# Optimization experiments

Hardware: AMD Instinct MI355X
Metric: run time of the kernel (lower is better)

The kernel has to match this reference:

```python
import jax, jax.numpy as jnp
import numpy as np

N = 50000
E = 800000
D_IN = 128
D_OUT = 128
LN_EPS = 1e-5
DROP_P = 0.1


def setup_inputs() -> dict:
    key = jax.random.key(0)
    ks = jax.random.split(key, 8)
    x = jax.random.normal(ks[0], (N, D_IN), dtype=jnp.float32)
    edge_index = jax.random.randint(ks[1], (2, E), 0, N, dtype=jnp.int64)
    # dropout mask: binary keep-mask scaled by 1/(1-p), as torch dropout produces
    u = jax.random.uniform(ks[2], (N, D_IN), dtype=jnp.float32)
    dropout_mask = (u > DROP_P).astype(jnp.float32) / (1.0 - DROP_P)
    # LayerNorm affine params
    gamma = jnp.ones((D_IN,), dtype=jnp.float32)
    beta = jnp.zeros((D_IN,), dtype=jnp.float32)
    # SAGEConv linears: lin_l (aggregated neighbors, with bias), lin_r (root, no bias)
    s = 1.0 / np.sqrt(D_IN)
    w_l = jax.random.uniform(ks[3], (D_OUT, D_IN), minval=-s, maxval=s, dtype=jnp.float32)
    b_l = jax.random.uniform(ks[4], (D_OUT,), minval=-s, maxval=s, dtype=jnp.float32)
    w_r = jax.random.uniform(ks[5], (D_OUT, D_IN), minval=-s, maxval=s, dtype=jnp.float32)
    return {"x": x, "edge_index": edge_index, "dropout_mask": dropout_mask,
            "gamma": gamma, "beta": beta, "w_l": w_l, "b_l": b_l, "w_r": w_r}


def reference(x, edge_index, dropout_mask, gamma, beta, w_l, b_l, w_r):
    # LayerNorm + ReLU + dropout mask
    mu = jnp.mean(x, axis=-1, keepdims=True)
    var = jnp.mean(jnp.square(x - mu), axis=-1, keepdims=True)
    h = (x - mu) * jax.lax.rsqrt(var + LN_EPS) * gamma + beta
    h = jax.nn.relu(h) * dropout_mask  # [N, D_IN]
    # SAGEConv: mean-aggregate source features into target nodes
    src = edge_index[0]
    dst = edge_index[1]
    msg = h[src]  # [E, D_IN] gathered messages
    agg = jax.ops.segment_sum(msg, dst, num_segments=N)  # [N, D_IN]
    deg = jax.ops.segment_sum(jnp.ones((E,), dtype=h.dtype), dst, num_segments=N)
    agg = agg / jnp.maximum(deg, 1.0)[:, None]
    # out = lin_l(agg) + lin_r(h)
    out = agg @ w_l.T + b_l + h @ w_r.T  # [N, D_OUT]
    return out
```

## Files before the change

### kernel.cpp

```cpp
#include <hip/hip_runtime.h>
#include <hip/hip_bf16.h>

#define N_NODES 50000
#define N_EDGES 800000
#define D 128
#define NB_SCAN ((N_NODES + 255) / 256)
#define NB_GEMM ((N_NODES + 63) / 64)
#define EDGES_PER_GEMM_BLOCK 1024

typedef short bf16x8 __attribute__((ext_vector_type(8)));
typedef float f32x4 __attribute__((ext_vector_type(4)));

__device__ __forceinline__ unsigned int bf16u(float f) {
  __hip_bfloat16 b = __float2bfloat16(f);
  return (unsigned int)*reinterpret_cast<unsigned short*>(&b);
}

__global__ __launch_bounds__(256) void zero_kernel(int* __restrict__ deg,
                                                   int* __restrict__ done) {
  const int i = blockIdx.x * 256 + threadIdx.x;
  if (i < N_NODES) deg[i] = 0;
  if (i == 0) *done = 0;
}

__global__ __launch_bounds__(256) void gemm_kernel(
    const float* __restrict__ x, const float* __restrict__ mask,
    const float* __restrict__ gamma, const float* __restrict__ beta,
    const float* __restrict__ w_l, const float* __restrict__ w_r,
    const float* __restrict__ b_l, unsigned int* __restrict__ gb,
    float* __restrict__ rp, const int* __restrict__ ei,
    int* __restrict__ deg, int* __restrict__ rank) {
  __shared__ unsigned short Bs[64 * 64 * 8];
  const int t = threadIdx.x;
  const int w = t >> 6;
  const int l = t & 63;
  const int lm = l & 15;
  const int quad = l >> 4;
  const int nb = blockIdx.x * 64;

  {
    const int e = blockIdx.x * EDGES_PER_GEMM_BLOCK + t * 4;
    if (e + 3 < N_EDGES) {
      const int4 d4 = *(const int4*)(ei + N_EDGES + e);
      int4 r4;
      r4.x = atomicAdd(&deg[d4.x], 1);
      r4.y = atomicAdd(&deg[d4.y], 1);
      r4.z = atomicAdd(&deg[d4.z], 1);
      r4.w = atomicAdd(&deg[d4.w], 1);
      *(int4*)(rank + e) = r4;
    } else {
      for (int k = e; k < N_EDGES; ++k)
        rank[k] = atomicAdd(&deg[ei[N_EDGES + k]], 1);
    }
  }

#pragma unroll
  for (int i = 0; i < 16; ++i) {
    const int fid = w * 16 + i;
    const int sub = fid >> 2;
    const int ch = fid & 3;
    const float* srcw = (sub < 8) ? (w_l + (size_t)(sub * 16 + lm) * D)
                                  : (w_r + (size_t)((sub - 8) * 16 + lm) * D);
    const float4 a = *(const float4*)(srcw + ch * 32 + quad * 8);
    const float4 b = *(const float4*)(srcw + ch * 32 + quad * 8 + 4);
    uint4 v;
    v.x = (bf16u(a.y) << 16) | bf16u(a.x);
    v.y = (bf16u(a.w) << 16) | bf16u(a.z);
    v.z = (bf16u(b.y) << 16) | bf16u(b.x);
    v.w = (bf16u(b.w) << 16) | bf16u(b.z);
    *(uint4*)(Bs + ((size_t)fid * 64 + l) * 8) = v;
  }

  int anode = nb + w * 16 + lm;
  if (anode >= N_NODES) anode = N_NODES - 1;
  const float* xrow = x + (size_t)anode * D;
  float xv[32];
  float s = 0.f, q = 0.f;
#pragma unroll
  for (int ch = 0; ch < 4; ++ch) {
    const float4 a = *(const float4*)(xrow + ch * 32 + quad * 8);
    const float4 b = *(const float4*)(xrow + ch * 32 + quad * 8 + 4);
    xv[ch * 8 + 0] = a.x; xv[ch * 8 + 1] = a.y;
    xv[ch * 8 + 2] = a.z; xv[ch * 8 + 3] = a.w;
    xv[ch * 8 + 4] = b.x; xv[ch * 8 + 5] = b.y;
    xv[ch * 8 + 6] = b.z; xv[ch * 8 + 7] = b.w;
    s += (a.x + a.y) + (a.z + a.w) + (b.x + b.y) + (b.z + b.w);
    q += a.x * a.x + a.y * a.y + a.z * a.z + a.w * a.w +
         b.x * b.x + b.y * b.y + b.z * b.z + b.w * b.w;
  }
  s += __shfl_xor(s, 16);
  s += __shfl_xor(s, 32);
  q += __shfl_xor(q, 16);
  q += __shfl_xor(q, 32);
  const float mean = s * (1.0f / 128.0f);
  const float var = q * (1.0f / 128.0f) - mean * mean;
  const float rs = rsqrtf(var + 1e-5f);

  const float* mrow = mask + (size_t)anode * D;
  bf16x8 af[4];
#pragma unroll
  for (int ch = 0; ch < 4; ++ch) {
    const int c0 = ch * 32 + quad * 8;
    const float4 g0 = *(const float4*)(gamma + c0);
    const float4 g1 = *(const float4*)(gamma + c0 + 4);
    const float4 b0 = *(const float4*)(beta + c0);
    const float4 b1 = *(const float4*)(beta + c0 + 4);
    const float4 m0 = *(const float4*)(mrow + c0);
    const float4 m1 = *(const float4*)(mrow + c0 + 4);
    const float gv[8] = {g0.x, g0.y, g0.z, g0.w, g1.x, g1.y, g1.z, g1.w};
    const float bv[8] = {b0.x, b0.y, b0.z, b0.w, b1.x, b1.y, b1.z, b1.w};
    const float mv[8] = {m0.x, m0.y, m0.z, m0.w, m1.x, m1.y, m1.z, m1.w};
#pragma unroll
    for (int j = 0; j < 8; ++j) {
      const float hv =
          fmaxf((xv[ch * 8 + j] - mean) * rs * gv[j] + bv[j], 0.0f) * mv[j];
      af[ch][j] = (short)bf16u(hv);
    }
  }
  __syncthreads();

  f32x4 acc[16];
#pragma unroll
  for (int sub = 0; sub < 16; ++sub) acc[sub] = (f32x4){0.f, 0.f, 0.f, 0.f};
  const bf16x8* BsF = (const bf16x8*)Bs;
#pragma unroll
  for (int sub = 0; sub < 16; ++sub)
#pragma unroll
    for (int ch = 0; ch < 4; ++ch)
      acc[sub] = __builtin_amdgcn_mfma_f32_16x16x32_bf16(
          af[ch], BsF[(sub * 4 + ch) * 64 + l], acc[sub], 0, 0, 0);

  float blv[8];
#pragma unroll
  for (int j = 0; j < 8; ++j) blv[j] = b_l[j * 16 + lm];

  const int node0 = nb + w * 16 + quad * 4;
#pragma unroll
  for (int reg = 0; reg < 4; ++reg) {
    const int node = node0 + reg;
    if (node < N_NODES) {
      uint4 p;
      p.x = (bf16u(acc[1][reg]) << 16) | bf16u(acc[0][reg]);
      p.y = (bf16u(acc[3][reg]) << 16) | bf16u(acc[2][reg]);
      p.z = (bf16u(acc[5][reg]) << 16) | bf16u(acc[4][reg]);
      p.w = (bf16u(acc[7][reg]) << 16) | bf16u(acc[6][reg]);
      ((uint4*)gb)[(size_t)node * 16 + lm] = p;
      float4 q0, q1;
      q0.x = acc[8][reg] + blv[0];
      q0.y = acc[9][reg] + blv[1];
      q0.z = acc[10][reg] + blv[2];
      q0.w = acc[11][reg] + blv[3];
      q1.x = acc[12][reg] + blv[4];
      q1.y = acc[13][reg] + blv[5];
      q1.z = acc[14][reg] + blv[6];
      q1.w = acc[15][reg] + blv[7];
      ((float4*)rp)[(size_t)node * 32 + lm * 2 + 0] = q0;
      ((float4*)rp)[(size_t)node * 32 + lm * 2 + 1] = q1;
    }
  }
}

__global__ __launch_bounds__(256) void scan12_kernel(
    const int* __restrict__ deg, int* __restrict__ offL1,
    int* __restrict__ partial, int* __restrict__ partial2,
    int* __restrict__ done) {
  __shared__ int sm[256];
  __shared__ int amLast;
  const int t = threadIdx.x;
  const int i = blockIdx.x * 256 + t;
  const int v = (i < N_NODES) ? deg[i] : 0;
  sm[t] = v;
  __syncthreads();
#pragma unroll
  for (int ofs = 1; ofs < 256; ofs <<= 1) {
    int x = sm[t];
    if (t >= ofs) x += sm[t - ofs];
    __syncthreads();
    sm[t] = x;
    __syncthreads();
  }
  if (i < N_NODES) offL1[i] = sm[t] - v;
  if (t == 255)
    __hip_atomic_store(&partial[blockIdx.x], sm[255], __ATOMIC_RELEASE,
                       __HIP_MEMORY_SCOPE_AGENT);
  __syncthreads();
  if (t == 0) amLast = (atomicAdd(done, 1) == gridDim.x - 1);
  __syncthreads();
  if (amLast) {
    const int pv = (t < NB_SCAN)
                       ? __hip_atomic_load(&partial[t], __ATOMIC_ACQUIRE,
                                           __HIP_MEMORY_SCOPE_AGENT)
                       : 0;
    sm[t] = pv;
    __syncthreads();
#pragma unroll
    for (int ofs = 1; ofs < 256; ofs <<= 1) {
      int x = sm[t];
      if (t >= ofs) x += sm[t - ofs];
      __syncthreads();
      sm[t] = x;
      __syncthreads();
    }
    if (t < NB_SCAN) partial2[t] = sm[t] - pv;
  }
}

__global__ __launch_bounds__(256) void scatter_kernel(
    const int* __restrict__ ei, const int* __restrict__ offL1,
    const int* __restrict__ partial2, const int* __restrict__ rank,
    int* __restrict__ csr) {
  const int e = (blockIdx.x * 256 + threadIdx.x) * 4;
  if (e + 3 < N_EDGES) {
    const int4 s4 = *(const int4*)(ei + e);
    const int4 d4 = *(const int4*)(ei + N_EDGES + e);
    const int4 r4 = *(const int4*)(rank + e);
    csr[offL1[d4.x] + partial2[d4.x >> 8] + r4.x] = s4.x;
    csr[offL1[d4.y] + partial2[d4.y >> 8] + r4.y] = s4.y;
    csr[offL1[d4.z] + partial2[d4.z >> 8] + r4.z] = s4.z;
    csr[offL1[d4.w] + partial2[d4.w >> 8] + r4.w] = s4.w;
  } else {
    for (int k = e; k < N_EDGES; ++k) {
      const int dst = ei[N_EDGES + k];
      csr[offL1[dst] + partial2[dst >> 8] + rank[k]] = ei[k];
    }
  }
}

#define ACC8(v)                                     \
  do {                                              \
    acc[0] += __uint_as_float((v).x << 16);         \
    acc[1] += __uint_as_float((v).x & 0xffff0000u); \
    acc[2] += __uint_as_float((v).y << 16);         \
    acc[3] += __uint_as_float((v).y & 0xffff0000u); \
    acc[4] += __uint_as_float((v).z << 16);         \
    acc[5] += __uint_as_float((v).z & 0xffff0000u); \
    acc[6] += __uint_as_float((v).w << 16);         \
    acc[7] += __uint_as_float((v).w & 0xffff0000u); \
  } while (0)

__global__ __launch_bounds__(256) void agg_kernel(
    const int* __restrict__ offL1, const int* __restrict__ partial2,
    const int* __restrict__ csr, const unsigned int* __restrict__ gb,
    const float* __restrict__ rp, float* __restrict__ out) {
  const int l = threadIdx.x & 63;
  const int q = l >> 4;
  const int c = l & 15;
  const int n = blockIdx.x * 4 + (threadIdx.x >> 6);
  const int s = offL1[n] + partial2[n >> 8];
  const int e = (n + 1 < N_NODES) ? offL1[n + 1] + partial2[(n + 1) >> 8]
                                  : N_EDGES;
  const uint4* g4 = (const uint4*)gb;
  float acc[8];
#pragma unroll
  for (int k = 0; k < 8; ++k) acc[k] = 0.0f;
  for (int base = s; base < e; base += 64) {
    const int cnt = min(e - base, 64);
    int idx = (l < cnt) ? csr[base + l] : 0;
    int j = 0;
    for (; j + 16 <= cnt; j += 16) {
      const int i0 = __shfl(idx, j + 0 + q);
      const int i1 = __shfl(idx, j + 4 + q);
      const int i2 = __shfl(idx, j + 8 + q);
      const int i3 = __shfl(idx, j + 12 + q);
      const uint4 v0 = g4[(size_t)i0 * 16 + c];
      const uint4 v1 = g4[(size_t)i1 * 16 + c];
      const uint4 v2 = g4[(size_t)i2 * 16 + c];
      const uint4 v3 = g4[(size_t)i3 * 16 + c];
      ACC8(v0);
      ACC8(v1);
      ACC8(v2);
      ACC8(v3);
    }
    for (; j + 4 <= cnt; j += 4) {
      const int i0 = __shfl(idx, j + q);
      const uint4 v0 = g4[(size_t)i0 * 16 + c];
      ACC8(v0);
    }
    if (j < cnt) {
      const int rem = cnt - j;
      const int i0 = __shfl(idx, j + min(q, rem - 1));
      if (q < rem) {
        const uint4 v0 = g4[(size_t)i0 * 16 + c];
        ACC8(v0);
      }
    }
  }
#pragma unroll
  for (int k = 0; k < 8; ++k) {
    acc[k] += __shfl_xor(acc[k], 16);
    acc[k] += __shfl_xor(acc[k], 32);
  }
  if (l < 16) {
    const float inv = 1.0f / fmaxf((float)(e - s), 1.0f);
    const float4 rp0 = ((const float4*)rp)[(size_t)n * 32 + c * 2 + 0];
    const float4 rp1 = ((const float4*)rp)[(size_t)n * 32 + c * 2 + 1];
    float* o = out + (size_t)n * D + c;
    o[0]   = fmaf(acc[0], inv, rp0.x);
    o[16]  = fmaf(acc[1], inv, rp0.y);
    o[32]  = fmaf(acc[2], inv, rp0.z);
    o[48]  = fmaf(acc[3], inv, rp0.w);
    o[64]  = fmaf(acc[4], inv, rp1.x);
    o[80]  = fmaf(acc[5], inv, rp1.y);
    o[96]  = fmaf(acc[6], inv, rp1.z);
    o[112] = fmaf(acc[7], inv, rp1.w);
  }
}

extern "C" void kernel_launch(void* const* d_in, const int* in_sizes, int n_in,
                              void* d_out, int out_size, void* d_ws,
                              size_t ws_size, hipStream_t stream) {
  const float* x = (const float*)d_in[0];
  const int* ei = (const int*)d_in[1];
  const float* mask = (const float*)d_in[2];
  const float* gamma = (const float*)d_in[3];
  const float* beta = (const float*)d_in[4];
  const float* w_l = (const float*)d_in[5];
  const float* b_l = (const float*)d_in[6];
  const float* w_r = (const float*)d_in[7];
  float* out = (float*)d_out;

  char* ws = (char*)d_ws;
  size_t off = 0;
  auto alloc = [&](size_t bytes) {
    char* p = ws + off;
    off += (bytes + 255) & ~(size_t)255;
    return p;
  };
  unsigned int* gb =
      (unsigned int*)alloc((size_t)N_NODES * D * sizeof(unsigned short));
  float* rp = (float*)alloc((size_t)N_NODES * D * sizeof(float));
  int* deg = (int*)alloc((size_t)N_NODES * sizeof(int));
  int* offL1 = (int*)alloc((size_t)N_NODES * sizeof(int));
  int* partial = (int*)alloc((size_t)NB_SCAN * sizeof(int));
  int* partial2 = (int*)alloc((size_t)NB_SCAN * sizeof(int));
  int* done = (int*)alloc(sizeof(int));
  int* rank = (int*)alloc((size_t)N_EDGES * sizeof(int));
  int* csr = (int*)alloc((size_t)N_EDGES * sizeof(int));

  zero_kernel<<<NB_SCAN, 256, 0, stream>>>(deg, done);
  gemm_kernel<<<NB_GEMM, 256, 0, stream>>>(x, mask, gamma, beta, w_l, w_r,
                                           b_l, gb, rp, ei, deg, rank);
  scan12_kernel<<<NB_SCAN, 256, 0, stream>>>(deg, offL1, partial, partial2,
                                             done);
  scatter_kernel<<<(N_EDGES / 4 + 255) / 256, 256, 0, stream>>>(
      ei, offL1, partial2, rank, csr);
  agg_kernel<<<N_NODES / 4, 256, 0, stream>>>(offL1, partial2, csr, gb, rp,
                                              out);
}
```

Baseline: 211.0 us.

## Pre-convert weights once, drop LDS staging and per-edge rank buffer

```diff
diff --git a/kernel.cpp b/kernel.cpp
--- a/kernel.cpp
+++ b/kernel.cpp
@@ -16,47 +16,21 @@
   return (unsigned int)*reinterpret_cast<unsigned short*>(&b);
 }
 
-__global__ __launch_bounds__(256) void zero_kernel(int* __restrict__ deg,
-                                                   int* __restrict__ done) {
+__global__ __launch_bounds__(256) void prep_kernel(
+    const float* __restrict__ w_l, const float* __restrict__ w_r,
+    unsigned int* __restrict__ wb, int* __restrict__ deg,
+    int* __restrict__ cnt, int* __restrict__ done) {
   const int i = blockIdx.x * 256 + threadIdx.x;
-  if (i < N_NODES) deg[i] = 0;
+  if (i < N_NODES) {
+    deg[i] = 0;
+    cnt[i] = 0;
+  }
   if (i == 0) *done = 0;
-}
-
-__global__ __launch_bounds__(256) void gemm_kernel(
-    const float* __restrict__ x, const float* __restrict__ mask,
-    const float* __restrict__ gamma, const float* __restrict__ beta,
-    const float* __restrict__ w_l, const float* __restrict__ w_r,
-    const float* __restrict__ b_l, unsigned int* __restrict__ gb,
-    float* __restrict__ rp, const int* __restrict__ ei,
-    int* __restrict__ deg, int* __restrict__ rank) {
-  __shared__ unsigned short Bs[64 * 64 * 8];
-  const int t = threadIdx.x;
-  const int w = t >> 6;
-  const int l = t & 63;
-  const int lm = l & 15;
-  const int quad = l >> 4;
-  const int nb = blockIdx.x * 64;
-
-  {
-    const int e = blockIdx.x * EDGES_PER_GEMM_BLOCK + t * 4;
-    if (e + 3 < N_EDGES) {
-      const int4 d4 = *(const int4*)(ei + N_EDGES + e);
-      int4 r4;
-      r4.x = atomicAdd(&deg[d4.x], 1);
-      r4.y = atomicAdd(&deg[d4.y], 1);
-      r4.z = atomicAdd(&deg[d4.z], 1);
-      r4.w = atomicAdd(&deg[d4.w], 1);
-      *(int4*)(rank + e) = r4;
-    } else {
-      for (int k = e; k < N_EDGES; ++k)
-        rank[k] = atomicAdd(&deg[ei[N_EDGES + k]], 1);
-    }
-  }
-
-#pragma unroll
-  for (int i = 0; i < 16; ++i) {
-    const int fid = w * 16 + i;
+  if (i < 4096) {
+    const int fid = i >> 6;
+    const int l = i & 63;
+    const int lm = l & 15;
+    const int quad = l >> 4;
     const int sub = fid >> 2;
     const int ch = fid & 3;
     const float* srcw = (sub < 8) ? (w_l + (size_t)(sub * 16 + lm) * D)
@@ -68,7 +42,34 @@
     v.y = (bf16u(a.w) << 16) | bf16u(a.z);
     v.z = (bf16u(b.y) << 16) | bf16u(b.x);
     v.w = (bf16u(b.w) << 16) | bf16u(b.z);
-    *(uint4*)(Bs + ((size_t)fid * 64 + l) * 8) = v;
+    ((uint4*)wb)[(size_t)fid * 64 + l] = v;
+  }
+}
+
+__global__ __launch_bounds__(256, 4) void gemm_kernel(
+    const float* __restrict__ x, const float* __restrict__ mask,
+    const float* __restrict__ gamma, const float* __restrict__ beta,
+    const unsigned int* __restrict__ wb, const float* __restrict__ b_l,
+    unsigned int* __restrict__ gb, float* __restrict__ rp,
+    const int* __restrict__ ei, int* __restrict__ deg) {
+  const int t = threadIdx.x;
+  const int w = t >> 6;
+  const int l = t & 63;
+  const int lm = l & 15;
+  const int quad = l >> 4;
+  const int nb = blockIdx.x * 64;
+
+  {
+    const int e = blockIdx.x * EDGES_PER_GEMM_BLOCK + t * 4;
+    if (e + 3 < N_EDGES) {
+      const int4 d4 = *(const int4*)(ei + N_EDGES + e);
+      atomicAdd(&deg[d4.x], 1);
+      atomicAdd(&deg[d4.y], 1);
+      atomicAdd(&deg[d4.z], 1);
+      atomicAdd(&deg[d4.w], 1);
+    } else {
+      for (int k = e; k < N_EDGES; ++k) atomicAdd(&deg[ei[N_EDGES + k]], 1);
+    }
   }
 
   int anode = nb + w * 16 + lm;
@@ -117,12 +118,11 @@
       af[ch][j] = (short)bf16u(hv);
     }
   }
-  __syncthreads();
 
   f32x4 acc[16];
 #pragma unroll
   for (int sub = 0; sub < 16; ++sub) acc[sub] = (f32x4){0.f, 0.f, 0.f, 0.f};
-  const bf16x8* BsF = (const bf16x8*)Bs;
+  const bf16x8* BsF = (const bf16x8*)wb;
 #pragma unroll
   for (int sub = 0; sub < 16; ++sub)
 #pragma unroll
@@ -207,21 +207,25 @@
 
 __global__ __launch_bounds__(256) void scatter_kernel(
     const int* __restrict__ ei, const int* __restrict__ offL1,
-    const int* __restrict__ partial2, const int* __restrict__ rank,
+    const int* __restrict__ partial2, int* __restrict__ cnt,
     int* __restrict__ csr) {
   const int e = (blockIdx.x * 256 + threadIdx.x) * 4;
   if (e + 3 < N_EDGES) {
     const int4 s4 = *(const int4*)(ei + e);
     const int4 d4 = *(const int4*)(ei + N_EDGES + e);
-    const int4 r4 = *(const int4*)(rank + e);
-    csr[offL1[d4.x] + partial2[d4.x >> 8] + r4.x] = s4.x;
-    csr[offL1[d4.y] + partial2[d4.y >> 8] + r4.y] = s4.y;
-    csr[offL1[d4.z] + partial2[d4.z >> 8] + r4.z] = s4.z;
-    csr[offL1[d4.w] + partial2[d4.w >> 8] + r4.w] = s4.w;
+    const int rx = atomicAdd(&cnt[d4.x], 1);
+    const int ry = atomicAdd(&cnt[d4.y], 1);
+    const int rz = atomicAdd(&cnt[d4.z], 1);
+    const int rw = atomicAdd(&cnt[d4.w], 1);
+    csr[offL1[d4.x] + partial2[d4.x >> 8] + rx] = s4.x;
+    csr[offL1[d4.y] + partial2[d4.y >> 8] + ry] = s4.y;
+    csr[offL1[d4.z] + partial2[d4.z >> 8] + rz] = s4.z;
+    csr[offL1[d4.w] + partial2[d4.w >> 8] + rw] = s4.w;
   } else {
     for (int k = e; k < N_EDGES; ++k) {
       const int dst = ei[N_EDGES + k];
-      csr[offL1[dst] + partial2[dst >> 8] + rank[k]] = ei[k];
+      const int r = atomicAdd(&cnt[dst], 1);
+      csr[offL1[dst] + partial2[dst >> 8] + r] = ei[k];
     }
   }
 }
@@ -330,20 +334,21 @@
       (unsigned int*)alloc((size_t)N_NODES * D * sizeof(unsigned short));
   float* rp = (float*)alloc((size_t)N_NODES * D * sizeof(float));
   int* deg = (int*)alloc((size_t)N_NODES * sizeof(int));
+  int* cnt = (int*)alloc((size_t)N_NODES * sizeof(int));
   int* offL1 = (int*)alloc((size_t)N_NODES * sizeof(int));
   int* partial = (int*)alloc((size_t)NB_SCAN * sizeof(int));
   int* partial2 = (int*)alloc((size_t)NB_SCAN * sizeof(int));
   int* done = (int*)alloc(sizeof(int));
-  int* rank = (int*)alloc((size_t)N_EDGES * sizeof(int));
   int* csr = (int*)alloc((size_t)N_EDGES * sizeof(int));
-
-  zero_kernel<<<NB_SCAN, 256, 0, stream>>>(deg, done);
-  gemm_kernel<<<NB_GEMM, 256, 0, stream>>>(x, mask, gamma, beta, w_l, w_r,
-                                           b_l, gb, rp, ei, deg, rank);
+  unsigned int* wb = (unsigned int*)alloc((size_t)4096 * 16);
+
+  prep_kernel<<<NB_SCAN, 256, 0, stream>>>(w_l, w_r, wb, deg, cnt, done);
+  gemm_kernel<<<NB_GEMM, 256, 0, stream>>>(x, mask, gamma, beta, wb, b_l, gb,
+                                           rp, ei, deg);
   scan12_kernel<<<NB_SCAN, 256, 0, stream>>>(deg, offL1, partial, partial2,
                                              done);
   scatter_kernel<<<(N_EDGES / 4 + 255) / 256, 256, 0, stream>>>(
-      ei, offL1, partial2, rank, csr);
+      ei, offL1, partial2, cnt, csr);
   agg_kernel<<<N_NODES / 4, 256, 0, stream>>>(offL1, partial2, csr, gb, rp,
                                               out);
 }
```

New measurement: 250.0 us. 1.18x slower.
